# Performance work log

Measured on AMD Instinct MI355X. Metric: run time of the kernel, lower is better.

The kernel has to match this reference:

```python
import jax, jax.numpy as jnp
import numpy as np

N = 50000          # nodes
E = 1600000        # edges (avg degree 32)
F_IN = 1280        # ESM node feature dim
H = 128            # hidden (128x0e irreps)
G = 64             # graphs in batch
OUT = 2
SH0 = 0.5 / np.sqrt(np.pi)   # Y_00 under e3nn 'integral' normalization (constant; l=1,2 sh
                             # have zero CG coupling into 0e outputs, so only l=0 survives)
TP_NORM = SH0 / np.sqrt(H)   # path weight normalization 1/sqrt(fan_in), fan_in = mul_in1*mul_in2 = H*1


def _mean_aggregate(msg, dst, num_nodes):
    # scatter-mean of per-edge messages onto destination nodes (PyG aggr='mean')
    s = jax.ops.segment_sum(msg, dst, num_segments=num_nodes)
    cnt = jax.ops.segment_sum(jnp.ones((msg.shape[0],), msg.dtype), dst, num_segments=num_nodes)
    return s / jnp.maximum(cnt, 1.0)[:, None]


def _equivariant_conv(h, edge_index, tp_w):
    # EquivariantConv: gather x_j, tensor product with sh(edge_vec), scatter-mean.
    # edge_vec normalization is irrelevant for the surviving l=0 path (Y_00 is constant).
    src, dst = edge_index[0], edge_index[1]
    msg = (h[src] @ tp_w) * TP_NORM            # [E, H]
    return _mean_aggregate(msg, dst, h.shape[0])


def setup_inputs() -> dict:
    key = jax.random.key(0)
    ks = jax.random.split(key, 16)
    inp = {
        "x": jax.random.normal(ks[0], (N, F_IN), jnp.float32),
        "pos": jax.random.normal(ks[1], (N, 3), jnp.float32),
        "edge_index": jax.random.randint(ks[2], (2, E), 0, N),
        "batch": jnp.sort(jax.random.randint(ks[3], (N,), 0, G)),
        # lin_in (xavier-like scale)
        "lin_w": jax.random.normal(ks[4], (F_IN, H), jnp.float32) * (1.0 / np.sqrt(F_IN)),
        "lin_b": jnp.zeros((H,), jnp.float32),
        # FullyConnectedTensorProduct internal weights ~ N(0,1), shape [mul_in, mul_out]
        "tp_w1": jax.random.normal(ks[5], (H, H), jnp.float32),
        "tp_w2": jax.random.normal(ks[6], (H, H), jnp.float32),
        "tp_w3": jax.random.normal(ks[7], (H, H), jnp.float32),
        # classifier
        "c1w": jax.random.normal(ks[8], (H, H), jnp.float32) * (1.0 / np.sqrt(H)),
        "c1b": jnp.zeros((H,), jnp.float32),
        "c2w": jax.random.normal(ks[9], (H, H), jnp.float32) * (1.0 / np.sqrt(H)),
        "c2b": jnp.zeros((H,), jnp.float32),
        "c3w": jax.random.normal(ks[10], (H, OUT), jnp.float32) * (1.0 / np.sqrt(H)),
        "c3b": jnp.zeros((OUT,), jnp.float32),
    }
    return inp


def reference(x, pos, edge_index, batch, lin_w, lin_b, tp_w1, tp_w2, tp_w3,
              c1w, c1b, c2w, c2b, c3w, c3b):
    h = jax.nn.relu(x @ lin_w + lin_b)                    # lin_in + relu (dropout p=0, eval)
    h = jax.nn.relu(_equivariant_conv(h, edge_index, tp_w1))
    h = jax.nn.relu(_equivariant_conv(h, edge_index, tp_w2))
    h = _equivariant_conv(h, edge_index, tp_w3)           # no relu after conv3
    # global_mean_pool over graphs
    s = jax.ops.segment_sum(h, batch, num_segments=G)
    cnt = jax.ops.segment_sum(jnp.ones((h.shape[0],), h.dtype), batch, num_segments=G)
    z = s / jnp.maximum(cnt, 1.0)[:, None]                # [G, H]
    o = jax.nn.relu(z @ c1w + c1b)
    o = jax.nn.relu(o @ c2w + c2b)
    out = o @ c3w + c3b                                   # [G, OUT]
    return (out, z)
```

## Files before the change

kernel.cpp:

```cpp
#include <hip/hip_runtime.h>
#include <hip/hip_bf16.h>

typedef __bf16 bf16_t;
typedef bf16_t bf16x4 __attribute__((ext_vector_type(4)));
typedef bf16_t bf16x8 __attribute__((ext_vector_type(8)));
typedef float f32x4 __attribute__((ext_vector_type(4)));

static constexpr int N_NODES = 50000;
static constexpr int N_EDGES = 1600000;
static constexpr int FIN = 1280;
static constexpr int HD = 128;
static constexpr int NG = 64;
static constexpr float TP_NORM_F = 0.0249338908f;

__global__ __launch_bounds__(256) void k_prep_pos(const float* __restrict__ lin_w,
                                                  const float* __restrict__ tp1,
                                                  const float* __restrict__ tp2,
                                                  bf16_t* __restrict__ WtL,
                                                  bf16_t* __restrict__ Wt1,
                                                  bf16_t* __restrict__ Wt2,
                                                  float* __restrict__ pbuf,
                                                  float* __restrict__ gcnt,
                                                  const int* __restrict__ dst,
                                                  int* __restrict__ cnt,
                                                  int* __restrict__ pos) {
  const int PREP_BLOCKS = 768;
  if (blockIdx.x < PREP_BLOCKS) {
    int idx = blockIdx.x * 256 + threadIdx.x;
    const int totL = FIN * HD;
    const int tot1 = HD * HD;
    if (idx < totL) {
      int k = idx >> 7, n = idx & 127;
      WtL[n * FIN + k] = (bf16_t)lin_w[idx];
    } else if (idx < totL + tot1) {
      int j = idx - totL;
      int k = j >> 7, n = j & 127;
      Wt1[n * HD + k] = (bf16_t)(tp1[j] * TP_NORM_F);
    } else {
      int j = idx - totL - tot1;
      int k = j >> 7, n = j & 127;
      Wt2[n * HD + k] = (bf16_t)(tp2[j] * TP_NORM_F);
    }
    if (idx < NG * HD) pbuf[idx] = 0.f;
    if (idx < NG) gcnt[idx] = 0.f;
  } else {
    int e = (blockIdx.x - PREP_BLOCKS) * 256 + threadIdx.x;
    if (e < N_EDGES) pos[e] = atomicAdd(&cnt[dst[e]], 1);
  }
}

__global__ __launch_bounds__(256) void k_scan1(const int* __restrict__ cnt, int* __restrict__ bsum, int n) {
  __shared__ int s[256];
  int t = threadIdx.x;
  int i = blockIdx.x * 256 + t;
  s[t] = (i < n) ? cnt[i] : 0;
  __syncthreads();
  for (int d = 128; d > 0; d >>= 1) {
    if (t < d) s[t] += s[t + d];
    __syncthreads();
  }
  if (t == 0) bsum[blockIdx.x] = s[0];
}

__global__ __launch_bounds__(256) void k_scan2(int* __restrict__ bsum, int nb) {
  __shared__ int s[256];
  int t = threadIdx.x;
  int v = (t < nb) ? bsum[t] : 0;
  s[t] = v;
  __syncthreads();
  for (int d = 1; d < 256; d <<= 1) {
    int x = (t >= d) ? s[t - d] : 0;
    __syncthreads();
    s[t] += x;
    __syncthreads();
  }
  if (t < nb) bsum[t] = s[t] - v;
  if (t == 255) bsum[nb] = s[255];
}

__global__ __launch_bounds__(256) void k_scan3(const int* __restrict__ cnt, const int* __restrict__ bsum,
                                               int* __restrict__ off, int n) {
  __shared__ int s[256];
  int t = threadIdx.x;
  int i = blockIdx.x * 256 + t;
  int v = (i < n) ? cnt[i] : 0;
  s[t] = v;
  __syncthreads();
  for (int d = 1; d < 256; d <<= 1) {
    int x = (t >= d) ? s[t - d] : 0;
    __syncthreads();
    s[t] += x;
    __syncthreads();
  }
  if (i < n) off[i] = bsum[blockIdx.x] + s[t] - v;
  if (i == n - 1) off[n] = bsum[blockIdx.x] + s[t];
}

__global__ __launch_bounds__(256) void k_lin_fill(const float* __restrict__ A,
                                                  const bf16_t* __restrict__ Bt,
                                                  const float* __restrict__ bias,
                                                  bf16_t* __restrict__ C,
                                                  const int* __restrict__ srcE,
                                                  const int* __restrict__ dstE,
                                                  const int* __restrict__ offn,
                                                  const int* __restrict__ pos,
                                                  int* __restrict__ ssrc) {
  __shared__ bf16_t As[32 * 64];
  __shared__ bf16_t Bs[128 * 64];
  const int GB = (N_NODES + 31) / 32;
  if (blockIdx.x >= GB) {
    int e = (blockIdx.x - GB) * 256 + threadIdx.x;
    if (e < N_EDGES) ssrc[offn[dstE[e]] + pos[e]] = srcE[e];
    return;
  }
  const int M = N_NODES, K = FIN;
  const int t = threadIdx.x;
  const int wid = t >> 6;
  const int lane = t & 63;
  const int wn = wid * 32;
  const int l15 = lane & 15;
  const int quad = lane >> 4;
  const int rowBase = blockIdx.x * 32;

  f32x4 acc[2][2];
#pragma unroll
  for (int i = 0; i < 2; ++i)
#pragma unroll
    for (int j = 0; j < 2; ++j) {
      f32x4 z = {0.f, 0.f, 0.f, 0.f};
      acc[i][j] = z;
    }

  for (int k0 = 0; k0 < K; k0 += 64) {
#pragma unroll
    for (int i = 0; i < 2; ++i) {
      int idx = t + i * 256;
      int row = idx >> 4;
      int col4 = idx & 15;
      int gr = rowBase + row;
      float4 v = make_float4(0.f, 0.f, 0.f, 0.f);
      if (gr < M) v = *(const float4*)(A + (size_t)gr * K + k0 + col4 * 4);
      bf16x4 w;
      w[0] = (bf16_t)v.x; w[1] = (bf16_t)v.y; w[2] = (bf16_t)v.z; w[3] = (bf16_t)v.w;
      int c = col4 >> 1;
      int off = row * 64 + ((c ^ (row & 7)) << 3) + ((col4 & 1) << 2);
      *(bf16x4*)&As[off] = w;
    }
#pragma unroll
    for (int i = 0; i < 4; ++i) {
      int idx = t + i * 256;
      int row = idx >> 3;
      int c = idx & 7;
      bf16x8 v = *(const bf16x8*)(Bt + (size_t)row * K + k0 + c * 8);
      int off = row * 64 + ((c ^ (row & 7)) << 3);
      *(bf16x8*)&Bs[off] = v;
    }
    __syncthreads();
#pragma unroll
    for (int kk = 0; kk < 2; ++kk) {
      bf16x8 af[2], bfr[2];
      int k8 = kk * 4 + quad;
#pragma unroll
      for (int mi = 0; mi < 2; ++mi) {
        int row = mi * 16 + l15;
        af[mi] = *(const bf16x8*)&As[row * 64 + ((k8 ^ (row & 7)) << 3)];
      }
#pragma unroll
      for (int ni = 0; ni < 2; ++ni) {
        int row = wn + ni * 16 + l15;
        bfr[ni] = *(const bf16x8*)&Bs[row * 64 + ((k8 ^ (row & 7)) << 3)];
      }
#pragma unroll
      for (int mi = 0; mi < 2; ++mi)
#pragma unroll
        for (int ni = 0; ni < 2; ++ni)
          acc[mi][ni] = __builtin_amdgcn_mfma_f32_16x16x32_bf16(af[mi], bfr[ni], acc[mi][ni], 0, 0, 0);
    }
    __syncthreads();
  }

#pragma unroll
  for (int mi = 0; mi < 2; ++mi) {
#pragma unroll
    for (int ni = 0; ni < 2; ++ni) {
      int col = wn + ni * 16 + l15;
      float bv = bias[col];
#pragma unroll
      for (int r = 0; r < 4; ++r) {
        int row = mi * 16 + quad * 4 + r;
        int gr = rowBase + row;
        if (gr < M) {
          float v = acc[mi][ni][r] + bv;
          v = fmaxf(v, 0.f);
          C[(size_t)gr * HD + col] = (bf16_t)v;
        }
      }
    }
  }
}

__global__ __launch_bounds__(256) void k_conv_fused(const bf16_t* __restrict__ hin,
                                                    const int* __restrict__ ssrc,
                                                    const int* __restrict__ off,
                                                    const bf16_t* __restrict__ Bt,
                                                    bf16_t* __restrict__ hout, int n) {
  __shared__ bf16_t As[32 * 128];
  __shared__ bf16_t Bs[128 * 128];
  const int t = threadIdx.x;
  const int wid = t >> 6;
  const int lane = t & 63;
  const int g = lane >> 4;
  const int fl = lane & 15;
  const int rowBase = blockIdx.x * 32;

#pragma unroll
  for (int i = 0; i < 8; ++i) {
    int idx = t + i * 256;
    int row = idx >> 4;
    int cc = idx & 15;
    bf16x8 v = *(const bf16x8*)(Bt + (size_t)row * HD + cc * 8);
    int hh = cc >> 3, c = cc & 7;
    int ob = (row * 2 + hh) * 64 + ((c ^ (row & 7)) << 3);
    *(bf16x8*)&Bs[ob] = v;
  }

  const bf16_t* hp = hin + fl * 8;
  for (int i = 0; i < 8; ++i) {
    int localRow = wid * 8 + i;
    int node = rowBase + localRow;
    if (node >= n) break;
    int b = off[node], e = off[node + 1];
    int deg = e - b;
    int d64 = min(deg, 64);
    int idxr = (lane < deg) ? ssrc[b + lane] : 0;
    float acc[8];
#pragma unroll
    for (int j = 0; j < 8; ++j) acc[j] = 0.f;

    int j0 = 0;
    for (; j0 + 32 <= d64; j0 += 32) {
      int s[8];
#pragma unroll
      for (int k = 0; k < 8; ++k) s[k] = __shfl(idxr, j0 + 4 * k + g);
      bf16x8 v[8];
#pragma unroll
      for (int k = 0; k < 8; ++k) v[k] = *(const bf16x8*)(hp + (size_t)s[k] * HD);
#pragma unroll
      for (int k = 0; k < 8; ++k)
#pragma unroll
        for (int jj = 0; jj < 8; ++jj) acc[jj] += (float)v[k][jj];
    }
    for (; j0 + 8 <= d64; j0 += 8) {
      int s0 = __shfl(idxr, j0 + g);
      int s1 = __shfl(idxr, j0 + 4 + g);
      bf16x8 v0 = *(const bf16x8*)(hp + (size_t)s0 * HD);
      bf16x8 v1 = *(const bf16x8*)(hp + (size_t)s1 * HD);
#pragma unroll
      for (int jj = 0; jj < 8; ++jj) acc[jj] += (float)v0[jj] + (float)v1[jj];
    }
    if (j0 + 4 <= d64) {
      int s0 = __shfl(idxr, j0 + g);
      bf16x8 v0 = *(const bf16x8*)(hp + (size_t)s0 * HD);
#pragma unroll
      for (int jj = 0; jj < 8; ++jj) acc[jj] += (float)v0[jj];
      j0 += 4;
    }
    if (j0 + g < d64) {
      int s0 = __shfl(idxr, j0 + g);
      bf16x8 v0 = *(const bf16x8*)(hp + (size_t)s0 * HD);
#pragma unroll
      for (int jj = 0; jj < 8; ++jj) acc[jj] += (float)v0[jj];
    }
    for (int ii = b + 64; ii + g < e; ii += 4) {
      int s0 = ssrc[ii + g];
      bf16x8 v0 = *(const bf16x8*)(hp + (size_t)s0 * HD);
#pragma unroll
      for (int jj = 0; jj < 8; ++jj) acc[jj] += (float)v0[jj];
    }
#pragma unroll
    for (int j = 0; j < 8; ++j) {
      acc[j] += __shfl_xor(acc[j], 16);
      acc[j] += __shfl_xor(acc[j], 32);
    }
    if (g == 0) {
      float inv = (e > b) ? 1.f / (float)(e - b) : 0.f;
      bf16x8 o;
#pragma unroll
      for (int j = 0; j < 8; ++j) o[j] = (bf16_t)(acc[j] * inv);
      int hh = fl >> 3, c = fl & 7;
      int oa = (localRow * 2 + hh) * 64 + ((c ^ (localRow & 7)) << 3);
      *(bf16x8*)&As[oa] = o;
    }
  }
  __syncthreads();

  const int wn = wid * 32;
  const int l15 = lane & 15;
  const int quad = lane >> 4;
  f32x4 acc[2][2];
#pragma unroll
  for (int i = 0; i < 2; ++i)
#pragma unroll
    for (int j = 0; j < 2; ++j) {
      f32x4 z = {0.f, 0.f, 0.f, 0.f};
      acc[i][j] = z;
    }
#pragma unroll
  for (int kk = 0; kk < 4; ++kk) {
    int k16 = kk * 4 + quad;
    int hh = k16 >> 3, c = k16 & 7;
    bf16x8 af[2], bfr[2];
#pragma unroll
    for (int mi = 0; mi < 2; ++mi) {
      int row = mi * 16 + l15;
      af[mi] = *(const bf16x8*)&As[(row * 2 + hh) * 64 + ((c ^ (row & 7)) << 3)];
    }
#pragma unroll
    for (int ni = 0; ni < 2; ++ni) {
      int row = wn + ni * 16 + l15;
      bfr[ni] = *(const bf16x8*)&Bs[(row * 2 + hh) * 64 + ((c ^ (row & 7)) << 3)];
    }
#pragma unroll
    for (int mi = 0; mi < 2; ++mi)
#pragma unroll
      for (int ni = 0; ni < 2; ++ni)
        acc[mi][ni] = __builtin_amdgcn_mfma_f32_16x16x32_bf16(af[mi], bfr[ni], acc[mi][ni], 0, 0, 0);
  }

#pragma unroll
  for (int mi = 0; mi < 2; ++mi) {
#pragma unroll
    for (int ni = 0; ni < 2; ++ni) {
      int col = wn + ni * 16 + l15;
#pragma unroll
      for (int r = 0; r < 4; ++r) {
        int row = mi * 16 + quad * 4 + r;
        int gr = rowBase + row;
        if (gr < n) {
          float v = fmaxf(acc[mi][ni][r], 0.f);
          hout[(size_t)gr * HD + col] = (bf16_t)v;
        }
      }
    }
  }
}

__global__ __launch_bounds__(256) void k_aggregate(const bf16_t* __restrict__ h,
                                                   const int* __restrict__ ssrc,
                                                   const int* __restrict__ off,
                                                   bf16_t* __restrict__ agg, int n) {
  int node = blockIdx.x * 4 + (threadIdx.x >> 6);
  if (node >= n) return;
  int lane = threadIdx.x & 63;
  int g = lane >> 4;
  int fl = lane & 15;
  int b = off[node], e = off[node + 1];
  int deg = e - b;
  int d64 = min(deg, 64);
  int idxr = (lane < deg) ? ssrc[b + lane] : 0;
  float acc[8];
#pragma unroll
  for (int j = 0; j < 8; ++j) acc[j] = 0.f;
  const bf16_t* hp = h + fl * 8;

  int j0 = 0;
  for (; j0 + 32 <= d64; j0 += 32) {
    int s[8];
#pragma unroll
    for (int k = 0; k < 8; ++k) s[k] = __shfl(idxr, j0 + 4 * k + g);
    bf16x8 v[8];
#pragma unroll
    for (int k = 0; k < 8; ++k) v[k] = *(const bf16x8*)(hp + (size_t)s[k] * HD);
#pragma unroll
    for (int k = 0; k < 8; ++k)
#pragma unroll
      for (int jj = 0; jj < 8; ++jj) acc[jj] += (float)v[k][jj];
  }
  for (; j0 + 8 <= d64; j0 += 8) {
    int s0 = __shfl(idxr, j0 + g);
    int s1 = __shfl(idxr, j0 + 4 + g);
    bf16x8 v0 = *(const bf16x8*)(hp + (size_t)s0 * HD);
    bf16x8 v1 = *(const bf16x8*)(hp + (size_t)s1 * HD);
#pragma unroll
    for (int jj = 0; jj < 8; ++jj) acc[jj] += (float)v0[jj] + (float)v1[jj];
  }
  if (j0 + 4 <= d64) {
    int s0 = __shfl(idxr, j0 + g);
    bf16x8 v0 = *(const bf16x8*)(hp + (size_t)s0 * HD);
#pragma unroll
    for (int jj = 0; jj < 8; ++jj) acc[jj] += (float)v0[jj];
    j0 += 4;
  }
  if (j0 + g < d64) {
    int s0 = __shfl(idxr, j0 + g);
    bf16x8 v0 = *(const bf16x8*)(hp + (size_t)s0 * HD);
#pragma unroll
    for (int jj = 0; jj < 8; ++jj) acc[jj] += (float)v0[jj];
  }
  for (int i = b + 64; i + g < e; i += 4) {
    int s0 = ssrc[i + g];
    bf16x8 v0 = *(const bf16x8*)(hp + (size_t)s0 * HD);
#pragma unroll
    for (int jj = 0; jj < 8; ++jj) acc[jj] += (float)v0[jj];
  }

#pragma unroll
  for (int j = 0; j < 8; ++j) {
    acc[j] += __shfl_xor(acc[j], 16);
    acc[j] += __shfl_xor(acc[j], 32);
  }
  if (g == 0) {
    float inv = (e > b) ? 1.f / (float)(e - b) : 0.f;
    bf16x8 o;
#pragma unroll
    for (int j = 0; j < 8; ++j) o[j] = (bf16_t)(acc[j] * inv);
    *(bf16x8*)(agg + (size_t)node * HD + fl * 8) = o;
  }
}

__global__ __launch_bounds__(128) void k_pool(const bf16_t* __restrict__ agg, const int* __restrict__ batch,
                                              float* __restrict__ p, float* __restrict__ gcnt, int n) {
  int base = blockIdx.x * 64;
  if (base >= n) return;
  int t = threadIdx.x;
  int end = min(base + 64, n);
  float acc = 0.f;
  int curg = batch[base];
  int runStart = base;
  for (int i = base; i < end; ++i) {
    int g = batch[i];
    if (g != curg) {
      atomicAdd(&p[curg * HD + t], acc);
      if (t == 0) atomicAdd(&gcnt[curg], (float)(i - runStart));
      acc = 0.f; curg = g; runStart = i;
    }
    acc += (float)agg[(size_t)i * HD + t];
  }
  atomicAdd(&p[curg * HD + t], acc);
  if (t == 0) atomicAdd(&gcnt[curg], (float)(end - runStart));
}

__global__ __launch_bounds__(128) void k_head(const float* __restrict__ p, const float* __restrict__ gcnt,
                                              const float* __restrict__ w3,
                                              const float* __restrict__ c1w, const float* __restrict__ c1b,
                                              const float* __restrict__ c2w, const float* __restrict__ c2b,
                                              const float* __restrict__ c3w, const float* __restrict__ c3b,
                                              float* __restrict__ out) {
  __shared__ float sa[128], sb[128];
  int g = blockIdx.x, t = threadIdx.x;
  float inv = 1.f / fmaxf(gcnt[g], 1.f);
  sa[t] = p[g * HD + t] * inv;
  __syncthreads();
  float z = 0.f;
  for (int k = 0; k < HD; ++k) z += sa[k] * w3[k * HD + t];
  z *= TP_NORM_F;
  out[128 + g * HD + t] = z;
  sb[t] = z;
  __syncthreads();
  float o1 = c1b[t];
  for (int k = 0; k < HD; ++k) o1 += sb[k] * c1w[k * HD + t];
  o1 = fmaxf(o1, 0.f);
  __syncthreads();
  sa[t] = o1;
  __syncthreads();
  float o2 = c2b[t];
  for (int k = 0; k < HD; ++k) o2 += sa[k] * c2w[k * HD + t];
  o2 = fmaxf(o2, 0.f);
  __syncthreads();
  sb[t] = o2;
  __syncthreads();
  if (t < 2) {
    float o = c3b[t];
    for (int k = 0; k < HD; ++k) o += sb[k] * c3w[k * 2 + t];
    out[g * 2 + t] = o;
  }
}

extern "C" void kernel_launch(void* const* d_in, const int* in_sizes, int n_in,
                              void* d_out, int out_size, void* d_ws, size_t ws_size,
                              hipStream_t stream) {
  const float* x = (const float*)d_in[0];
  const int* eidx = (const int*)d_in[2];
  const int* src = eidx;
  const int* dst = eidx + N_EDGES;
  const int* batch = (const int*)d_in[3];
  const float* lin_w = (const float*)d_in[4];
  const float* lin_b = (const float*)d_in[5];
  const float* tp_w1 = (const float*)d_in[6];
  const float* tp_w2 = (const float*)d_in[7];
  const float* tp_w3 = (const float*)d_in[8];
  const float* c1w = (const float*)d_in[9];
  const float* c1b = (const float*)d_in[10];
  const float* c2w = (const float*)d_in[11];
  const float* c2b = (const float*)d_in[12];
  const float* c3w = (const float*)d_in[13];
  const float* c3b = (const float*)d_in[14];
  float* out = (float*)d_out;
  (void)in_sizes; (void)n_in; (void)out_size; (void)ws_size;

  uintptr_t wp = (uintptr_t)d_ws;
  auto alloc = [&](size_t bytes) -> void* {
    uintptr_t a = (wp + 255) & ~(uintptr_t)255;
    wp = a + bytes;
    return (void*)a;
  };
  bf16_t* WtL  = (bf16_t*)alloc(sizeof(bf16_t) * (size_t)HD * FIN);
  bf16_t* Wt1  = (bf16_t*)alloc(sizeof(bf16_t) * (size_t)HD * HD);
  bf16_t* Wt2  = (bf16_t*)alloc(sizeof(bf16_t) * (size_t)HD * HD);
  bf16_t* h    = (bf16_t*)alloc(sizeof(bf16_t) * (size_t)50048 * HD);
  bf16_t* agg  = (bf16_t*)alloc(sizeof(bf16_t) * (size_t)50048 * HD);
  int*    cnt  = (int*)alloc(sizeof(int) * N_NODES);
  int*    bsum = (int*)alloc(sizeof(int) * 256);
  int*    offs = (int*)alloc(sizeof(int) * (N_NODES + 1));
  int*    pos  = (int*)alloc(sizeof(int) * N_EDGES);
  int*    ssrc = (int*)alloc(sizeof(int) * N_EDGES);
  float*  pbuf = (float*)alloc(sizeof(float) * NG * HD);
  float*  gcnt = (float*)alloc(sizeof(float) * NG);

  hipMemsetAsync(cnt, 0, sizeof(int) * N_NODES, stream);

  const int posBlocks = (N_EDGES + 255) / 256;
  k_prep_pos<<<768 + posBlocks, 256, 0, stream>>>(lin_w, tp_w1, tp_w2, WtL, Wt1, Wt2,
                                                  pbuf, gcnt, dst, cnt, pos);

  const int nScanBlocks = (N_NODES + 255) / 256;
  k_scan1<<<nScanBlocks, 256, 0, stream>>>(cnt, bsum, N_NODES);
  k_scan2<<<1, 256, 0, stream>>>(bsum, nScanBlocks);
  k_scan3<<<nScanBlocks, 256, 0, stream>>>(cnt, bsum, offs, N_NODES);

  const int gblocks = (N_NODES + 31) / 32;
  k_lin_fill<<<gblocks + posBlocks, 256, 0, stream>>>(x, WtL, lin_b, h, src, dst, offs, pos, ssrc);

  k_conv_fused<<<gblocks, 256, 0, stream>>>(h, ssrc, offs, Wt1, agg, N_NODES);
  k_conv_fused<<<gblocks, 256, 0, stream>>>(agg, ssrc, offs, Wt2, h, N_NODES);
  k_aggregate<<<(N_NODES + 3) / 4, 256, 0, stream>>>(h, ssrc, offs, agg, N_NODES);

  k_pool<<<(N_NODES + 63) / 64, 128, 0, stream>>>(agg, batch, pbuf, gcnt, N_NODES);
  k_head<<<NG, 128, 0, stream>>>(pbuf, gcnt, tp_w3, c1w, c1b, c2w, c2b, c3w, c3b, out);
}
```

Measured before the change: 707.7 us.

## Sort CSR neighbor lists by source tile within each destination

```diff
diff --git a/kernel.cpp b/kernel.cpp
--- a/kernel.cpp
+++ b/kernel.cpp
@@ -13,17 +13,22 @@
 static constexpr int NG = 64;
 static constexpr float TP_NORM_F = 0.0249338908f;
 
-__global__ __launch_bounds__(256) void k_prep_pos(const float* __restrict__ lin_w,
-                                                  const float* __restrict__ tp1,
-                                                  const float* __restrict__ tp2,
-                                                  bf16_t* __restrict__ WtL,
-                                                  bf16_t* __restrict__ Wt1,
-                                                  bf16_t* __restrict__ Wt2,
-                                                  float* __restrict__ pbuf,
-                                                  float* __restrict__ gcnt,
-                                                  const int* __restrict__ dst,
-                                                  int* __restrict__ cnt,
-                                                  int* __restrict__ pos) {
+static constexpr int TILE_SH = 10;
+static constexpr int TPN = 49;
+static constexpr int NBUCK = N_NODES * TPN;
+
+__global__ __launch_bounds__(256) void k_prep_hist(const float* __restrict__ lin_w,
+                                                   const float* __restrict__ tp1,
+                                                   const float* __restrict__ tp2,
+                                                   bf16_t* __restrict__ WtL,
+                                                   bf16_t* __restrict__ Wt1,
+                                                   bf16_t* __restrict__ Wt2,
+                                                   float* __restrict__ pbuf,
+                                                   float* __restrict__ gcnt,
+                                                   const int* __restrict__ srcE,
+                                                   const int* __restrict__ dstE,
+                                                   int* __restrict__ bcnt,
+                                                   int* __restrict__ pos) {
   const int PREP_BLOCKS = 768;
   if (blockIdx.x < PREP_BLOCKS) {
     int idx = blockIdx.x * 256 + threadIdx.x;
@@ -45,7 +50,11 @@
     if (idx < NG) gcnt[idx] = 0.f;
   } else {
     int e = (blockIdx.x - PREP_BLOCKS) * 256 + threadIdx.x;
-    if (e < N_EDGES) pos[e] = atomicAdd(&cnt[dst[e]], 1);
+    if (e < N_EDGES) {
+      int s = srcE[e], d = dstE[e];
+      int key = d * TPN + (s >> TILE_SH);
+      pos[e] = atomicAdd(&bcnt[key], 1);
+    }
   }
 }
 
@@ -102,7 +111,7 @@
                                                   bf16_t* __restrict__ C,
                                                   const int* __restrict__ srcE,
                                                   const int* __restrict__ dstE,
-                                                  const int* __restrict__ offn,
+                                                  const int* __restrict__ boff,
                                                   const int* __restrict__ pos,
                                                   int* __restrict__ ssrc) {
   __shared__ bf16_t As[32 * 64];
@@ -110,7 +119,11 @@
   const int GB = (N_NODES + 31) / 32;
   if (blockIdx.x >= GB) {
     int e = (blockIdx.x - GB) * 256 + threadIdx.x;
-    if (e < N_EDGES) ssrc[offn[dstE[e]] + pos[e]] = srcE[e];
+    if (e < N_EDGES) {
+      int s = srcE[e], d = dstE[e];
+      int key = d * TPN + (s >> TILE_SH);
+      ssrc[boff[key] + pos[e]] = s;
+    }
     return;
   }
   const int M = N_NODES, K = FIN;
@@ -201,7 +214,7 @@
 
 __global__ __launch_bounds__(256) void k_conv_fused(const bf16_t* __restrict__ hin,
                                                     const int* __restrict__ ssrc,
-                                                    const int* __restrict__ off,
+                                                    const int* __restrict__ boff,
                                                     const bf16_t* __restrict__ Bt,
                                                     bf16_t* __restrict__ hout, int n) {
   __shared__ bf16_t As[32 * 128];
@@ -229,7 +242,7 @@
     int localRow = wid * 8 + i;
     int node = rowBase + localRow;
     if (node >= n) break;
-    int b = off[node], e = off[node + 1];
+    int b = boff[node * TPN], e = boff[node * TPN + TPN];
     int deg = e - b;
     int d64 = min(deg, 64);
     int idxr = (lane < deg) ? ssrc[b + lane] : 0;
@@ -347,14 +360,14 @@
 
 __global__ __launch_bounds__(256) void k_aggregate(const bf16_t* __restrict__ h,
                                                    const int* __restrict__ ssrc,
-                                                   const int* __restrict__ off,
+                                                   const int* __restrict__ boff,
                                                    bf16_t* __restrict__ agg, int n) {
   int node = blockIdx.x * 4 + (threadIdx.x >> 6);
   if (node >= n) return;
   int lane = threadIdx.x & 63;
   int g = lane >> 4;
   int fl = lane & 15;
-  int b = off[node], e = off[node + 1];
+  int b = boff[node * TPN], e = boff[node * TPN + TPN];
   int deg = e - b;
   int d64 = min(deg, 64);
   int idxr = (lane < deg) ? ssrc[b + lane] : 0;
@@ -509,31 +522,36 @@
   bf16_t* Wt2  = (bf16_t*)alloc(sizeof(bf16_t) * (size_t)HD * HD);
   bf16_t* h    = (bf16_t*)alloc(sizeof(bf16_t) * (size_t)50048 * HD);
   bf16_t* agg  = (bf16_t*)alloc(sizeof(bf16_t) * (size_t)50048 * HD);
-  int*    cnt  = (int*)alloc(sizeof(int) * N_NODES);
-  int*    bsum = (int*)alloc(sizeof(int) * 256);
-  int*    offs = (int*)alloc(sizeof(int) * (N_NODES + 1));
+  int*    bcnt = (int*)alloc(sizeof(int) * NBUCK);
+  int*    boff = (int*)alloc(sizeof(int) * (NBUCK + 1));
+  int*    bsumA= (int*)alloc(sizeof(int) * 9600);
+  int*    bsumB= (int*)alloc(sizeof(int) * 300);
+  int*    boffA= (int*)alloc(sizeof(int) * 9600);
   int*    pos  = (int*)alloc(sizeof(int) * N_EDGES);
   int*    ssrc = (int*)alloc(sizeof(int) * N_EDGES);
   float*  pbuf = (float*)alloc(sizeof(float) * NG * HD);
   float*  gcnt = (float*)alloc(sizeof(float) * NG);
 
-  hipMemsetAsync(cnt, 0, sizeof(int) * N_NODES, stream);
-
-  const int posBlocks = (N_EDGES + 255) / 256;
-  k_prep_pos<<<768 + posBlocks, 256, 0, stream>>>(lin_w, tp_w1, tp_w2, WtL, Wt1, Wt2,
-                                                  pbuf, gcnt, dst, cnt, pos);
-
-  const int nScanBlocks = (N_NODES + 255) / 256;
-  k_scan1<<<nScanBlocks, 256, 0, stream>>>(cnt, bsum, N_NODES);
-  k_scan2<<<1, 256, 0, stream>>>(bsum, nScanBlocks);
-  k_scan3<<<nScanBlocks, 256, 0, stream>>>(cnt, bsum, offs, N_NODES);
+  hipMemsetAsync(bcnt, 0, sizeof(int) * NBUCK, stream);
+
+  const int edgeBlocks = (N_EDGES + 255) / 256;
+  k_prep_hist<<<768 + edgeBlocks, 256, 0, stream>>>(lin_w, tp_w1, tp_w2, WtL, Wt1, Wt2,
+                                                    pbuf, gcnt, src, dst, bcnt, pos);
+
+  const int L1 = (NBUCK + 255) / 256;
+  const int L2 = (L1 + 255) / 256;
+  k_scan1<<<L1, 256, 0, stream>>>(bcnt, bsumA, NBUCK);
+  k_scan1<<<L2, 256, 0, stream>>>(bsumA, bsumB, L1);
+  k_scan2<<<1, 256, 0, stream>>>(bsumB, L2);
+  k_scan3<<<L2, 256, 0, stream>>>(bsumA, bsumB, boffA, L1);
+  k_scan3<<<L1, 256, 0, stream>>>(bcnt, boffA, boff, NBUCK);
 
   const int gblocks = (N_NODES + 31) / 32;
-  k_lin_fill<<<gblocks + posBlocks, 256, 0, stream>>>(x, WtL, lin_b, h, src, dst, offs, pos, ssrc);
-
-  k_conv_fused<<<gblocks, 256, 0, stream>>>(h, ssrc, offs, Wt1, agg, N_NODES);
-  k_conv_fused<<<gblocks, 256, 0, stream>>>(agg, ssrc, offs, Wt2, h, N_NODES);
-  k_aggregate<<<(N_NODES + 3) / 4, 256, 0, stream>>>(h, ssrc, offs, agg, N_NODES);
+  k_lin_fill<<<gblocks + edgeBlocks, 256, 0, stream>>>(x, WtL, lin_b, h, src, dst, boff, pos, ssrc);
+
+  k_conv_fused<<<gblocks, 256, 0, stream>>>(h, ssrc, boff, Wt1, agg, N_NODES);
+  k_conv_fused<<<gblocks, 256, 0, stream>>>(agg, ssrc, boff, Wt2, h, N_NODES);
+  k_aggregate<<<(N_NODES + 3) / 4, 256, 0, stream>>>(h, ssrc, boff, agg, N_NODES);
 
   k_pool<<<(N_NODES + 63) / 64, 128, 0, stream>>>(agg, batch, pbuf, gcnt, N_NODES);
   k_head<<<NG, 128, 0, stream>>>(pbuf, gcnt, tp_w3, c1w, c1b, c2w, c2b, c3w, c3b, out);
```

New measurement: 719.0 us. About the same (+1.6%).

## Split input GEMM across histogram and scan kernels to overlap CSR build

Applied to the files above, without the earlier changes.

```diff
diff --git a/kernel.cpp b/kernel.cpp
--- a/kernel.cpp
+++ b/kernel.cpp
@@ -13,106 +13,47 @@
 static constexpr int NG = 64;
 static constexpr float TP_NORM_F = 0.0249338908f;
 
-__global__ __launch_bounds__(256) void k_prep_pos(const float* __restrict__ lin_w,
-                                                  const float* __restrict__ tp1,
-                                                  const float* __restrict__ tp2,
-                                                  bf16_t* __restrict__ WtL,
-                                                  bf16_t* __restrict__ Wt1,
-                                                  bf16_t* __restrict__ Wt2,
-                                                  float* __restrict__ pbuf,
-                                                  float* __restrict__ gcnt,
-                                                  const int* __restrict__ dst,
-                                                  int* __restrict__ cnt,
-                                                  int* __restrict__ pos) {
-  const int PREP_BLOCKS = 768;
-  if (blockIdx.x < PREP_BLOCKS) {
-    int idx = blockIdx.x * 256 + threadIdx.x;
-    const int totL = FIN * HD;
-    const int tot1 = HD * HD;
-    if (idx < totL) {
-      int k = idx >> 7, n = idx & 127;
-      WtL[n * FIN + k] = (bf16_t)lin_w[idx];
-    } else if (idx < totL + tot1) {
-      int j = idx - totL;
-      int k = j >> 7, n = j & 127;
-      Wt1[n * HD + k] = (bf16_t)(tp1[j] * TP_NORM_F);
-    } else {
-      int j = idx - totL - tot1;
-      int k = j >> 7, n = j & 127;
-      Wt2[n * HD + k] = (bf16_t)(tp2[j] * TP_NORM_F);
-    }
-    if (idx < NG * HD) pbuf[idx] = 0.f;
-    if (idx < NG) gcnt[idx] = 0.f;
-  } else {
-    int e = (blockIdx.x - PREP_BLOCKS) * 256 + threadIdx.x;
-    if (e < N_EDGES) pos[e] = atomicAdd(&cnt[dst[e]], 1);
-  }
-}
-
-__global__ __launch_bounds__(256) void k_scan1(const int* __restrict__ cnt, int* __restrict__ bsum, int n) {
-  __shared__ int s[256];
-  int t = threadIdx.x;
-  int i = blockIdx.x * 256 + t;
-  s[t] = (i < n) ? cnt[i] : 0;
-  __syncthreads();
-  for (int d = 128; d > 0; d >>= 1) {
-    if (t < d) s[t] += s[t + d];
-    __syncthreads();
-  }
-  if (t == 0) bsum[blockIdx.x] = s[0];
-}
-
-__global__ __launch_bounds__(256) void k_scan2(int* __restrict__ bsum, int nb) {
-  __shared__ int s[256];
-  int t = threadIdx.x;
-  int v = (t < nb) ? bsum[t] : 0;
-  s[t] = v;
-  __syncthreads();
-  for (int d = 1; d < 256; d <<= 1) {
-    int x = (t >= d) ? s[t - d] : 0;
-    __syncthreads();
-    s[t] += x;
-    __syncthreads();
-  }
-  if (t < nb) bsum[t] = s[t] - v;
-  if (t == 255) bsum[nb] = s[255];
-}
-
-__global__ __launch_bounds__(256) void k_scan3(const int* __restrict__ cnt, const int* __restrict__ bsum,
-                                               int* __restrict__ off, int n) {
-  __shared__ int s[256];
-  int t = threadIdx.x;
-  int i = blockIdx.x * 256 + t;
-  int v = (i < n) ? cnt[i] : 0;
-  s[t] = v;
-  __syncthreads();
-  for (int d = 1; d < 256; d <<= 1) {
-    int x = (t >= d) ? s[t - d] : 0;
-    __syncthreads();
-    s[t] += x;
-    __syncthreads();
-  }
-  if (i < n) off[i] = bsum[blockIdx.x] + s[t] - v;
-  if (i == n - 1) off[n] = bsum[blockIdx.x] + s[t];
-}
-
-__global__ __launch_bounds__(256) void k_lin_fill(const float* __restrict__ A,
-                                                  const bf16_t* __restrict__ Bt,
-                                                  const float* __restrict__ bias,
-                                                  bf16_t* __restrict__ C,
-                                                  const int* __restrict__ srcE,
-                                                  const int* __restrict__ dstE,
-                                                  const int* __restrict__ offn,
-                                                  const int* __restrict__ pos,
-                                                  int* __restrict__ ssrc) {
+static constexpr int EB = (N_EDGES + 255) / 256;
+static constexpr int SC = (N_NODES + 255) / 256;
+static constexpr int GB = (N_NODES + 31) / 32;
+static constexpr int SL_A = 520, SL_B = 520, SL_C = 260, SL_D = GB - SL_A - SL_B - SL_C;
+
+__global__ __launch_bounds__(256) void k_prep(const float* __restrict__ lin_w,
+                                              const float* __restrict__ tp1,
+                                              const float* __restrict__ tp2,
+                                              bf16_t* __restrict__ WtL,
+                                              bf16_t* __restrict__ Wt1,
+                                              bf16_t* __restrict__ Wt2,
+                                              float* __restrict__ pbuf,
+                                              float* __restrict__ gcnt,
+                                              int* __restrict__ cnt) {
+  int idx = blockIdx.x * 256 + threadIdx.x;
+  const int totL = FIN * HD;
+  const int tot1 = HD * HD;
+  if (idx < totL) {
+    int k = idx >> 7, n = idx & 127;
+    WtL[n * FIN + k] = (bf16_t)lin_w[idx];
+  } else if (idx < totL + tot1) {
+    int j = idx - totL;
+    int k = j >> 7, n = j & 127;
+    Wt1[n * HD + k] = (bf16_t)(tp1[j] * TP_NORM_F);
+  } else if (idx < totL + 2 * tot1) {
+    int j = idx - totL - tot1;
+    int k = j >> 7, n = j & 127;
+    Wt2[n * HD + k] = (bf16_t)(tp2[j] * TP_NORM_F);
+  }
+  if (idx < NG * HD) pbuf[idx] = 0.f;
+  if (idx < NG) gcnt[idx] = 0.f;
+  if (idx < N_NODES) cnt[idx] = 0;
+}
+
+__device__ __forceinline__ void gemm_tile(const float* __restrict__ A,
+                                          const bf16_t* __restrict__ Bt,
+                                          const float* __restrict__ bias,
+                                          bf16_t* __restrict__ C,
+                                          int rowBase) {
   __shared__ bf16_t As[32 * 64];
   __shared__ bf16_t Bs[128 * 64];
-  const int GB = (N_NODES + 31) / 32;
-  if (blockIdx.x >= GB) {
-    int e = (blockIdx.x - GB) * 256 + threadIdx.x;
-    if (e < N_EDGES) ssrc[offn[dstE[e]] + pos[e]] = srcE[e];
-    return;
-  }
   const int M = N_NODES, K = FIN;
   const int t = threadIdx.x;
   const int wid = t >> 6;
@@ -120,7 +61,6 @@
   const int wn = wid * 32;
   const int l15 = lane & 15;
   const int quad = lane >> 4;
-  const int rowBase = blockIdx.x * 32;
 
   f32x4 acc[2][2];
 #pragma unroll
@@ -197,6 +137,109 @@
       }
     }
   }
+}
+
+__device__ __forceinline__ void scan1_body(const int* __restrict__ cnt, int* __restrict__ bsum,
+                                           int n, int blk) {
+  __shared__ int s1[256];
+  int t = threadIdx.x;
+  int i = blk * 256 + t;
+  s1[t] = (i < n) ? cnt[i] : 0;
+  __syncthreads();
+  for (int d = 128; d > 0; d >>= 1) {
+    if (t < d) s1[t] += s1[t + d];
+    __syncthreads();
+  }
+  if (t == 0) bsum[blk] = s1[0];
+}
+
+__device__ __forceinline__ void scan2_body(int* __restrict__ bsum, int nb) {
+  __shared__ int s2[256];
+  int t = threadIdx.x;
+  int v = (t < nb) ? bsum[t] : 0;
+  s2[t] = v;
+  __syncthreads();
+  for (int d = 1; d < 256; d <<= 1) {
+    int x = (t >= d) ? s2[t - d] : 0;
+    __syncthreads();
+    s2[t] += x;
+    __syncthreads();
+  }
+  if (t < nb) bsum[t] = s2[t] - v;
+}
+
+__device__ __forceinline__ void scan3_body(const int* __restrict__ cnt, const int* __restrict__ bsum,
+                                           int* __restrict__ off, int* __restrict__ woff,
+                                           int n, int blk) {
+  __shared__ int s3[256];
+  int t = threadIdx.x;
+  int i = blk * 256 + t;
+  int v = (i < n) ? cnt[i] : 0;
+  s3[t] = v;
+  __syncthreads();
+  for (int d = 1; d < 256; d <<= 1) {
+    int x = (t >= d) ? s3[t - d] : 0;
+    __syncthreads();
+    s3[t] += x;
+    __syncthreads();
+  }
+  if (i < n) {
+    int o = bsum[blk] + s3[t] - v;
+    off[i] = o;
+    woff[i] = o;
+  }
+  if (i == n - 1) off[n] = bsum[blk] + s3[t];
+}
+
+__global__ __launch_bounds__(256) void k_hist_gemm(const int* __restrict__ dstE, int* __restrict__ cnt,
+                                                   const float* __restrict__ x, const bf16_t* __restrict__ WtL,
+                                                   const float* __restrict__ lin_b, bf16_t* __restrict__ h) {
+  if (blockIdx.x < EB) {
+    int e = blockIdx.x * 256 + threadIdx.x;
+    if (e < N_EDGES) atomicAdd(&cnt[dstE[e]], 1);
+  } else {
+    gemm_tile(x, WtL, lin_b, h, (int)(blockIdx.x - EB) * 32);
+  }
+}
+
+__global__ __launch_bounds__(256) void k_scan1_gemm(const int* __restrict__ cnt, int* __restrict__ bsum,
+                                                    const float* __restrict__ x, const bf16_t* __restrict__ WtL,
+                                                    const float* __restrict__ lin_b, bf16_t* __restrict__ h) {
+  if (blockIdx.x < SC) {
+    scan1_body(cnt, bsum, N_NODES, blockIdx.x);
+  } else {
+    gemm_tile(x, WtL, lin_b, h, (SL_A + (int)(blockIdx.x - SC)) * 32);
+  }
+}
+
+__global__ __launch_bounds__(256) void k_scan2_gemm(int* __restrict__ bsum,
+                                                    const float* __restrict__ x, const bf16_t* __restrict__ WtL,
+                                                    const float* __restrict__ lin_b, bf16_t* __restrict__ h) {
+  if (blockIdx.x < 1) {
+    scan2_body(bsum, SC);
+  } else {
+    gemm_tile(x, WtL, lin_b, h, (SL_A + SL_B + (int)(blockIdx.x - 1)) * 32);
+  }
+}
+
+__global__ __launch_bounds__(256) void k_scan3_gemm(const int* __restrict__ cnt, const int* __restrict__ bsum,
+                                                    int* __restrict__ off, int* __restrict__ woff,
+                                                    const float* __restrict__ x, const bf16_t* __restrict__ WtL,
+                                                    const float* __restrict__ lin_b, bf16_t* __restrict__ h) {
+  if (blockIdx.x < SC) {
+    scan3_body(cnt, bsum, off, woff, N_NODES, blockIdx.x);
+  } else {
+    gemm_tile(x, WtL, lin_b, h, (SL_A + SL_B + SL_C + (int)(blockIdx.x - SC)) * 32);
+  }
+}
+
+__global__ __launch_bounds__(256) void k_fill(const int* __restrict__ srcE, const int* __restrict__ dstE,
+                                              int* __restrict__ woff, int* __restrict__ ssrc) {
+  int e = blockIdx.x * 256 + threadIdx.x;
+  if (e >= N_EDGES) return;
+  int s = srcE[e];
+  int slot = atomicAdd(&woff[dstE[e]], 1);
+  ssrc[slot] = s;
 }
 
 __global__ __launch_bounds__(256) void k_conv_fused(const bf16_t* __restrict__ hin,
@@ -512,27 +555,22 @@
   int*    cnt  = (int*)alloc(sizeof(int) * N_NODES);
   int*    bsum = (int*)alloc(sizeof(int) * 256);
   int*    offs = (int*)alloc(sizeof(int) * (N_NODES + 1));
-  int*    pos  = (int*)alloc(sizeof(int) * N_EDGES);
+  int*    woff = (int*)alloc(sizeof(int) * N_NODES);
   int*    ssrc = (int*)alloc(sizeof(int) * N_EDGES);
   float*  pbuf = (float*)alloc(sizeof(float) * NG * HD);
   float*  gcnt = (float*)alloc(sizeof(float) * NG);
 
-  hipMemsetAsync(cnt, 0, sizeof(int) * N_NODES, stream);
-
-  const int posBlocks = (N_EDGES + 255) / 256;
-  k_prep_pos<<<768 + posBlocks, 256, 0, stream>>>(lin_w, tp_w1, tp_w2, WtL, Wt1, Wt2,
-                                                  pbuf, gcnt, dst, cnt, pos);
-
-  const int nScanBlocks = (N_NODES + 255) / 256;
-  k_scan1<<<nScanBlocks, 256, 0, stream>>>(cnt, bsum, N_NODES);
-  k_scan2<<<1, 256, 0, stream>>>(bsum, nScanBlocks);
-  k_scan3<<<nScanBlocks, 256, 0, stream>>>(cnt, bsum, offs, N_NODES);
-
-  const int gblocks = (N_NODES + 31) / 32;
-  k_lin_fill<<<gblocks + posBlocks, 256, 0, stream>>>(x, WtL, lin_b, h, src, dst, offs, pos, ssrc);
-
-  k_conv_fused<<<gblocks, 256, 0, stream>>>(h, ssrc, offs, Wt1, agg, N_NODES);
-  k_conv_fused<<<gblocks, 256, 0, stream>>>(agg, ssrc, offs, Wt2, h, N_NODES);
+  k_prep<<<768, 256, 0, stream>>>(lin_w, tp_w1, tp_w2, WtL, Wt1, Wt2, pbuf, gcnt, cnt);
+
+  k_hist_gemm<<<EB + SL_A, 256, 0, stream>>>(dst, cnt, x, WtL, lin_b, h);
+  k_scan1_gemm<<<SC + SL_B, 256, 0, stream>>>(cnt, bsum, x, WtL, lin_b, h);
+  k_scan2_gemm<<<1 + SL_C, 256, 0, stream>>>(bsum, x, WtL, lin_b, h);
+  k_scan3_gemm<<<SC + SL_D, 256, 0, stream>>>(cnt, bsum, offs, woff, x, WtL, lin_b, h);
+
+  k_fill<<<EB, 256, 0, stream>>>(src, dst, woff, ssrc);
+
+  k_conv_fused<<<GB, 256, 0, stream>>>(h, ssrc, offs, Wt1, agg, N_NODES);
+  k_conv_fused<<<GB, 256, 0, stream>>>(agg, ssrc, offs, Wt2, h, N_NODES);
   k_aggregate<<<(N_NODES + 3) / 4, 256, 0, stream>>>(h, ssrc, offs, agg, N_NODES);
 
   k_pool<<<(N_NODES + 63) / 64, 128, 0, stream>>>(agg, batch, pbuf, gcnt, N_NODES);
```

New measurement: 860.1 us. 1.22x slower.
